# Kernel tuning notes

Measured on AMD Instinct MI355X. Metric: run time of the kernel, lower is better.

The kernel has to match this reference:

```python
import jax, jax.numpy as jnp
import numpy as np

TOP_K = 6  # num_experts_per_tok


def _glu_mlp(x, wg, wu, wd):
    # DeepSeek MLP: down( silu(gate(x)) * up(x) )
    return (jax.nn.silu(x @ wg) * (x @ wu)) @ wd


def setup_inputs() -> dict:
    key = jax.random.key(0)
    ks = jax.random.split(key, 8)
    B, S, D, E, F, FS = 2, 2048, 1024, 8, 512, 1024
    sc = 0.02
    return {
        "hidden_states": jax.random.normal(ks[0], (B, S, D), jnp.float32),
        "router_w": jax.random.normal(ks[1], (D, E), jnp.float32) * sc,
        "w_gate": jax.random.normal(ks[2], (E, D, F), jnp.float32) * sc,
        "w_up": jax.random.normal(ks[3], (E, D, F), jnp.float32) * sc,
        "w_down": jax.random.normal(ks[4], (E, F, D), jnp.float32) * sc,
        "ws_gate": jax.random.normal(ks[5], (D, FS), jnp.float32) * sc,
        "ws_up": jax.random.normal(ks[6], (D, FS), jnp.float32) * sc,
        "ws_down": jax.random.normal(ks[7], (FS, D), jnp.float32) * sc,
    }


def reference(hidden_states, router_w, w_gate, w_up, w_down, ws_gate, ws_up, ws_down):
    B, S, D = hidden_states.shape
    x = hidden_states.reshape(-1, D)                       # [T, D] tokens
    # Gate: softmax router + top-k (DeepSeek gate, no renorm)
    scores = jax.nn.softmax(x @ router_w, axis=-1)         # [T, E]
    topk_w, topk_idx = jax.lax.top_k(scores, TOP_K)        # [T, K]
    # Expert SiLU-GLU MLPs evaluated for all experts (math-identical to the
    # argsort dispatch -> grouped GEMM -> scatter combine in moe_infer)
    g = jnp.einsum('td,edf->etf', x, w_gate)               # [E, T, F]
    u = jnp.einsum('td,edf->etf', x, w_up)                 # [E, T, F]
    f_all = jnp.einsum('etf,efd->ted', jax.nn.silu(g) * u, w_down)  # [T, E, D]
    # Combine: final[t] = sum_k topk_w[t,k] * expert_{topk_idx[t,k]}(x[t])
    picked = jnp.take_along_axis(f_all, topk_idx[:, :, None], axis=1)  # [T, K, D]
    y = jnp.sum(picked * topk_w[:, :, None], axis=1).reshape(B, S, D)
    # shared experts branch
    y = y + _glu_mlp(hidden_states, ws_gate, ws_up, ws_down)
    return y
```

## Files before the change

### kernel.cpp

```cpp
#include <hip/hip_runtime.h>

typedef __attribute__((ext_vector_type(8))) short bf16x8;
typedef __attribute__((ext_vector_type(8))) unsigned short ushort8;
typedef __attribute__((ext_vector_type(4))) float floatx4;

static __device__ __forceinline__ unsigned short f2b(float f) {
  union { float f; unsigned int i; } v; v.f = f;
  unsigned int x = v.i;
  return (unsigned short)((x + 0x7fffu + ((x >> 16) & 1u)) >> 16);
}

#define GLDS(gp, lp) \
  __builtin_amdgcn_global_load_lds( \
      (const __attribute__((address_space(1))) unsigned int*)(gp), \
      (__attribute__((address_space(3))) unsigned int*)(lp), 16, 0, 0)

static __device__ __forceinline__ void swizzle_mn(int lin, int Mb, int Nb,
                                                  int& m_idx, int& n_idx) {
  if ((Mb & 7) == 0) {
    int xcd = lin & 7;
    int idx = lin >> 3;
    int nstrips = Mb >> 3;
    m_idx = (idx % nstrips) * 8 + xcd;
    n_idx = idx / nstrips;
  } else {
    m_idx = lin % Mb;
    n_idx = lin / Mb;
  }
}

__global__ __launch_bounds__(256) void router_cvt(
    const float* __restrict__ X, const float* __restrict__ RW,
    float* __restrict__ cw, unsigned short* __restrict__ Xb) {
  const int tid = threadIdx.x;
  const int wid = tid >> 6, lane = tid & 63;
  const int t = blockIdx.x * 4 + wid;
  const float* xp = X + (size_t)t * 1024;
  unsigned short* xo = Xb + (size_t)t * 1024;
  float acc[8];
#pragma unroll
  for (int e = 0; e < 8; e++) acc[e] = 0.f;
#pragma unroll
  for (int i = 0; i < 4; i++) {
    const int d0 = i * 256 + lane * 4;
    float4 v = *(const float4*)(xp + d0);
    ushort4 o;
    o.x = f2b(v.x); o.y = f2b(v.y); o.z = f2b(v.z); o.w = f2b(v.w);
    *(ushort4*)(xo + d0) = o;
    const float xv[4] = {v.x, v.y, v.z, v.w};
#pragma unroll
    for (int j = 0; j < 4; j++) {
      const float* r = RW + (size_t)(d0 + j) * 8;
      float4 r0 = *(const float4*)r;
      float4 r1 = *(const float4*)(r + 4);
      acc[0] += xv[j] * r0.x; acc[1] += xv[j] * r0.y;
      acc[2] += xv[j] * r0.z; acc[3] += xv[j] * r0.w;
      acc[4] += xv[j] * r1.x; acc[5] += xv[j] * r1.y;
      acc[6] += xv[j] * r1.z; acc[7] += xv[j] * r1.w;
    }
  }
#pragma unroll
  for (int m = 1; m < 64; m <<= 1) {
#pragma unroll
    for (int e = 0; e < 8; e++) acc[e] += __shfl_xor(acc[e], m);
  }
  if (lane == 0) {
    float mx = acc[0];
#pragma unroll
    for (int e = 1; e < 8; e++) mx = fmaxf(mx, acc[e]);
    float prob[8], s = 0.f;
#pragma unroll
    for (int e = 0; e < 8; e++) { prob[e] = expf(acc[e] - mx); s += prob[e]; }
    float inv = 1.f / s;
#pragma unroll
    for (int e = 0; e < 8; e++) prob[e] *= inv;
    int m1 = 0;
#pragma unroll
    for (int e = 1; e < 8; e++) if (prob[e] < prob[m1]) m1 = e;
    int m2 = -1;
#pragma unroll
    for (int e = 0; e < 8; e++)
      if (e != m1 && (m2 < 0 || prob[e] < prob[m2])) m2 = e;
#pragma unroll
    for (int e = 0; e < 8; e++)
      cw[(size_t)t * 8 + e] = (e == m1 || e == m2) ? 0.f : prob[e];
  }
}

__global__ __launch_bounds__(256) void transpose_all(
    const float* __restrict__ wg, const float* __restrict__ wu,
    const float* __restrict__ wd, const float* __restrict__ wsg,
    const float* __restrict__ wsu, const float* __restrict__ wsd,
    unsigned short* __restrict__ wgT, unsigned short* __restrict__ wuT,
    unsigned short* __restrict__ wdT, unsigned short* __restrict__ wsgT,
    unsigned short* __restrict__ wsuT, unsigned short* __restrict__ wsdT) {
  __shared__ __align__(16) unsigned short T[64 * 68];
  const int z = blockIdx.z;
  const float* src; unsigned short* dst; int K, N;
  if (z < 8)       { src = wg  + (size_t)z * 1024 * 512;        dst = wgT + (size_t)z * 512 * 1024;        K = 1024; N = 512; }
  else if (z < 16) { src = wu  + (size_t)(z - 8) * 1024 * 512;  dst = wuT + (size_t)(z - 8) * 512 * 1024;  K = 1024; N = 512; }
  else if (z < 24) { src = wd  + (size_t)(z - 16) * 512 * 1024; dst = wdT + (size_t)(z - 16) * 1024 * 512; K = 512;  N = 1024; }
  else if (z == 24){ src = wsg; dst = wsgT; K = 1024; N = 1024; }
  else if (z == 25){ src = wsu; dst = wsuT; K = 1024; N = 1024; }
  else             { src = wsd; dst = wsdT; K = 1024; N = 1024; }
  const int bn = blockIdx.x * 64, bk = blockIdx.y * 64;
  if (bn >= N || bk >= K) return;
  const int tid = threadIdx.x;
  {
    const int r = tid >> 4;
    const int c = (tid & 15) * 4;
#pragma unroll
    for (int i = 0; i < 4; i++) {
      const int rr = r + i * 16;
      float4 v = *(const float4*)(src + (size_t)(bk + rr) * N + bn + c);
      ushort4 o;
      o.x = f2b(v.x); o.y = f2b(v.y); o.z = f2b(v.z); o.w = f2b(v.w);
      *(ushort4*)(&T[rr * 68 + c]) = o;
    }
  }
  __syncthreads();
  {
    const int n_ = tid >> 3;
    const int k0 = (tid & 7) * 8;
#pragma unroll
    for (int p = 0; p < 2; p++) {
      const int n = n_ + p * 32;
      ushort8 o;
#pragma unroll
      for (int j = 0; j < 8; j++) o[j] = T[(k0 + j) * 68 + n];
      *(ushort8*)(dst + (size_t)(bn + n) * K + bk + k0) = o;
    }
  }
}

#define VMCNT(N) asm volatile("s_waitcnt vmcnt(" #N ")" ::: "memory")
#define BARS() do { __builtin_amdgcn_s_barrier(); \
                    __builtin_amdgcn_sched_barrier(0); } while (0)

#define STG_I0(K, BS) do { \
  GLDS(a0 + (K),          sm + (BS) + wid * 512); \
  GLDS(a0 + (K) + 131072, sm + (BS) + 8192 + wid * 512); } while (0)
#define STG_I1(K, BS) do { \
  GLDS(bg0 + (K),        sm + (BS) + 16384 + wid * 1024); \
  GLDS(bg0 + (K) + 8192, sm + (BS) + 16384 + wid * 1024 + 512); } while (0)
#define STG_I2(K, BS) do { \
  GLDS(bu0 + (K),        sm + (BS) + 24576 + wid * 1024); \
  GLDS(bu0 + (K) + 8192, sm + (BS) + 24576 + wid * 1024 + 512); } while (0)
#define STG_I3(K, BS) do { \
  GLDS(a0 + (K) + 65536,  sm + (BS) + 4096 + wid * 512); \
  GLDS(a0 + (K) + 196608, sm + (BS) + 12288 + wid * 512); } while (0)

#define READ_A(DST, DB, H) do { _Pragma("unroll") \
  for (int mf = 0; mf < 4; ++mf) { \
    const int row_ = wm * 128 + (H) * 64 + mf * 16 + lr; \
    const int rb_ = (DB) + row_ * 64; const int rx_ = row_ & 7; \
    DST[mf][0] = *(const bf16x8*)(sm + rb_ + ((quad ^ rx_) << 3)); \
    DST[mf][1] = *(const bf16x8*)(sm + rb_ + (((4 + quad) ^ rx_) << 3)); \
  } } while (0)

#define READ_B(DST, DB, RG) do { _Pragma("unroll") \
  for (int nf = 0; nf < 2; ++nf) { \
    const int row_ = wn * 32 + nf * 16 + lr; \
    const int rb_ = (DB) + (RG) + row_ * 64; const int rx_ = row_ & 7; \
    DST[nf][0] = *(const bf16x8*)(sm + rb_ + ((quad ^ rx_) << 3)); \
    DST[nf][1] = *(const bf16x8*)(sm + rb_ + (((4 + quad) ^ rx_) << 3)); \
  } } while (0)

#define MM(ACC, AF, BF) do { \
  __builtin_amdgcn_s_setprio(1); \
  _Pragma("unroll") \
  for (int mf = 0; mf < 4; ++mf) { _Pragma("unroll") \
    for (int nf = 0; nf < 2; ++nf) { \
      ACC[mf][nf] = __builtin_amdgcn_mfma_f32_16x16x32_bf16( \
          AF[mf][0], BF[nf][0], ACC[mf][nf], 0, 0, 0); \
      ACC[mf][nf] = __builtin_amdgcn_mfma_f32_16x16x32_bf16( \
          AF[mf][1], BF[nf][1], ACC[mf][nf], 0, 0, 0); \
    } } \
  __builtin_amdgcn_s_setprio(0); } while (0)

__global__ __launch_bounds__(512, 2) void gemm_gu_fused(
    const unsigned short* __restrict__ X,
    const unsigned short* __restrict__ WgTe,
    const unsigned short* __restrict__ WgTs,
    const unsigned short* __restrict__ WuTe,
    const unsigned short* __restrict__ WuTs,
    unsigned short* __restrict__ H,
    const float* __restrict__ cw, int Mb) {
  __shared__ __align__(16) unsigned short sm[65536];
  const int tid = threadIdx.x;
  const int wid = tid >> 6, lane = tid & 63;
  const int lr = lane & 15, quad = lane >> 4;
  const int wm = wid >> 2, wn = wid & 3;

  int m_idx, n_idx;
  {
    const int lin = blockIdx.x;
    const int xcd = lin & 7;
    const int idx = lin >> 3;
    m_idx = idx / 5;
    n_idx = xcd * 5 + (idx - m_idx * 5);
  }
  const int m0 = m_idx * 256;
  const int n0 = n_idx * 128;

  const unsigned short *Bg, *Bu;
  int eidx = -1;
  if (n0 < 4096) {
    eidx = n0 >> 9;
    size_t off = ((size_t)eidx * 512 + (n0 & 511)) * 1024;
    Bg = WgTe + off; Bu = WuTe + off;
  } else {
    size_t off = (size_t)(n0 - 4096) * 1024;
    Bg = WgTs + off; Bu = WuTs + off;
  }

  const int grow8 = lane >> 3;
  const int gcol = ((lane & 7) ^ grow8) << 3;
  const unsigned short* a0 =
      X + (size_t)(m0 + wid * 8 + grow8) * 1024 + gcol;
  const unsigned short* bg0 =
      Bg + (size_t)(wid * 16 + grow8) * 1024 + gcol;
  const unsigned short* bu0 =
      Bu + (size_t)(wid * 16 + grow8) * 1024 + gcol;

  floatx4 gg[2][4][2], uu[2][4][2];
#pragma unroll
  for (int h = 0; h < 2; h++)
#pragma unroll
    for (int mf = 0; mf < 4; mf++)
#pragma unroll
      for (int nf = 0; nf < 2; nf++) {
        gg[h][mf][nf] = (floatx4)0.f;
        uu[h][mf][nf] = (floatx4)0.f;
      }

  bf16x8 fA0[4][2], fA1[4][2], fBg[2][2], fBu[2][2];

  STG_I0(0, 0); STG_I1(0, 0); STG_I2(0, 0); STG_I3(0, 0);

  for (int t = 0; t < 15; ++t) {
    const int db = (t & 1) << 15;
    const int nb = 32768 - db;
    const int kn = (t + 1) * 64;
    STG_I0(kn, nb);
    VMCNT(6); BARS();
    READ_A(fA0, db, 0);
    READ_B(fBg, db, 16384);
    MM(gg[0], fA0, fBg);
    STG_I1(kn, nb);
    VMCNT(6); BARS();
    READ_B(fBu, db, 24576);
    MM(uu[0], fA0, fBu);
    STG_I2(kn, nb);
    VMCNT(6); BARS();
    READ_A(fA1, db, 1);
    MM(gg[1], fA1, fBg);
    STG_I3(kn, nb);
    BARS();
    MM(uu[1], fA1, fBu);
  }
  {
    const int db = 32768;
    VMCNT(4); BARS();
    READ_A(fA0, db, 0);
    READ_B(fBg, db, 16384);
    MM(gg[0], fA0, fBg);
    VMCNT(2); BARS();
    READ_B(fBu, db, 24576);
    MM(uu[0], fA0, fBu);
    VMCNT(0); BARS();
    READ_A(fA1, db, 1);
    MM(gg[1], fA1, fBg);
    MM(uu[1], fA1, fBu);
  }

#pragma unroll
  for (int h = 0; h < 2; h++) {
#pragma unroll
    for (int mf = 0; mf < 4; mf++) {
#pragma unroll
      for (int nf = 0; nf < 2; nf++) {
#pragma unroll
        for (int r = 0; r < 4; r++) {
          int row = m0 + wm * 128 + h * 64 + mf * 16 + quad * 4 + r;
          int col = n0 + wn * 32 + nf * 16 + lr;
          float g = gg[h][mf][nf][r];
          float u = uu[h][mf][nf][r];
          float s = (eidx >= 0) ? cw[(size_t)row * 8 + eidx] : 1.0f;
          float silu = g / (1.0f + __expf(-g));
          H[(size_t)row * 5120 + col] = f2b(s * silu * u);
        }
      }
    }
  }
}

#define DN_STG(KN, SBUF) do { \
  GLDS(Ha + (size_t)(KN),          smD + (SBUF) + wid * 512); \
  GLDS(Ha + (size_t)(KN) + 327680, smD + (SBUF) + 4096 + wid * 512); \
  const unsigned short *b0p_, *b1p_; \
  if ((KN) < 4096) { \
    const unsigned short* be_ = WdTe + ((size_t)((KN) >> 9)) * (1024 * 512) + ((KN) & 511); \
    b0p_ = be_ + (size_t)bn0 * 512 + gcol; \
    b1p_ = be_ + (size_t)(bn0 + 64) * 512 + gcol; \
  } else { \
    b0p_ = WdTs + (size_t)bn0 * 1024 + ((KN) - 4096) + gcol; \
    b1p_ = WdTs + (size_t)(bn0 + 64) * 1024 + ((KN) - 4096) + gcol; \
  } \
  GLDS(b0p_, smD + (SBUF) + 8192 + wid * 512); \
  GLDS(b1p_, smD + (SBUF) + 12288 + wid * 512); } while (0)

#define DN_TILE(T, BUF, SBUF, DOSTG, VM) do { \
  VMCNT(VM); BARS(); \
  if (DOSTG) { DN_STG(((T) + 3) * 64, SBUF); } \
  bf16x8 af_[4][2], bf_[2][2]; \
  _Pragma("unroll") \
  for (int mt = 0; mt < 4; ++mt) { \
    const int row_ = wm * 64 + mt * 16 + lr; \
    const int rb_ = (BUF) + row_ * 64; const int rx_ = row_ & 7; \
    af_[mt][0] = *(const bf16x8*)(smD + rb_ + ((quad ^ rx_) << 3)); \
    af_[mt][1] = *(const bf16x8*)(smD + rb_ + (((4 + quad) ^ rx_) << 3)); \
  } \
  _Pragma("unroll") \
  for (int nt = 0; nt < 2; ++nt) { \
    const int row_ = wn * 32 + nt * 16 + lr; \
    const int rb_ = (BUF) + 8192 + row_ * 64; const int rx_ = row_ & 7; \
    bf_[nt][0] = *(const bf16x8*)(smD + rb_ + ((quad ^ rx_) << 3)); \
    bf_[nt][1] = *(const bf16x8*)(smD + rb_ + (((4 + quad) ^ rx_) << 3)); \
  } \
  __builtin_amdgcn_s_setprio(1); \
  _Pragma("unroll") \
  for (int kt = 0; kt < 2; ++kt) \
    _Pragma("unroll") \
    for (int mt = 0; mt < 4; ++mt) \
      _Pragma("unroll") \
      for (int nt = 0; nt < 2; ++nt) \
        acc[mt][nt] = __builtin_amdgcn_mfma_f32_16x16x32_bf16( \
            af_[mt][kt], bf_[nt][kt], acc[mt][nt], 0, 0, 0); \
  __builtin_amdgcn_s_setprio(0); } while (0)

__global__ __launch_bounds__(512, 2) void gemm_down(
    const unsigned short* __restrict__ H,
    const unsigned short* __restrict__ WdTe,
    const unsigned short* __restrict__ WdTs,
    float* __restrict__ Y, int Mb) {
  __shared__ __align__(16) unsigned short smD[65536];
  const int tid = threadIdx.x;
  const int wid = tid >> 6, lane = tid & 63;
  const int lr = lane & 15, quad = lane >> 4;
  const int wm = wid >> 2, wn = wid & 3;
  int m_idx, n_idx;
  swizzle_mn(blockIdx.x, Mb, 8, m_idx, n_idx);
  const int m0 = m_idx * 128;
  const int n0 = n_idx * 128;

  const int grow8 = lane >> 3;
  const int gcol = ((lane & 7) ^ grow8) << 3;
  const unsigned short* Ha = H + (size_t)(m0 + wid * 8 + grow8) * 5120 + gcol;
  const int bn0 = n0 + wid * 8 + grow8;

  floatx4 acc[4][2];
#pragma unroll
  for (int i = 0; i < 4; i++)
#pragma unroll
    for (int j = 0; j < 2; j++) acc[i][j] = (floatx4)0.f;

  DN_STG(0, 0);
  DN_STG(64, 16384);
  DN_STG(128, 32768);

  for (int t = 0; t < 76; t += 4) {
    DN_TILE(t,     0,     49152, true, 8);
    DN_TILE(t + 1, 16384, 0,     true, 8);
    DN_TILE(t + 2, 32768, 16384, true, 8);
    DN_TILE(t + 3, 49152, 32768, true, 8);
  }
  DN_TILE(76, 0,     49152, true,  8);
  DN_TILE(77, 16384, 0,     false, 8);
  DN_TILE(78, 32768, 0,     false, 4);
  DN_TILE(79, 49152, 0,     false, 0);

#pragma unroll
  for (int mt = 0; mt < 4; mt++)
#pragma unroll
    for (int nt = 0; nt < 2; nt++)
#pragma unroll
      for (int r = 0; r < 4; r++) {
        int row = m0 + wm * 64 + mt * 16 + quad * 4 + r;
        int col = n0 + wn * 32 + nt * 16 + lr;
        Y[(size_t)row * 1024 + col] = acc[mt][nt][r];
      }
}

extern "C" void kernel_launch(void* const* d_in, const int* in_sizes, int n_in,
                              void* d_out, int out_size, void* d_ws, size_t ws_size,
                              hipStream_t stream) {
  const float* hs  = (const float*)d_in[0];
  const float* rw  = (const float*)d_in[1];
  const float* wg  = (const float*)d_in[2];
  const float* wu  = (const float*)d_in[3];
  const float* wd  = (const float*)d_in[4];
  const float* wsg = (const float*)d_in[5];
  const float* wsu = (const float*)d_in[6];
  const float* wsd = (const float*)d_in[7];
  float* out = (float*)d_out;

  char* p = (char*)d_ws;
  float* cw = (float*)p;                    p += (size_t)4096 * 8 * 4;
  unsigned short* Xb   = (unsigned short*)p; p += (size_t)4096 * 1024 * 2;
  unsigned short* wgT  = (unsigned short*)p; p += (size_t)8 * 512 * 1024 * 2;
  unsigned short* wuT  = (unsigned short*)p; p += (size_t)8 * 512 * 1024 * 2;
  unsigned short* wsgT = (unsigned short*)p; p += (size_t)1024 * 1024 * 2;
  unsigned short* wsuT = (unsigned short*)p; p += (size_t)1024 * 1024 * 2;
  unsigned short* wdT  = (unsigned short*)p; p += (size_t)8 * 1024 * 512 * 2;
  unsigned short* wsdT = (unsigned short*)p; p += (size_t)1024 * 1024 * 2;
  unsigned short* GH   = (unsigned short*)p;
  const size_t base_bytes = (size_t)(p - (char*)d_ws);

  int chunks = 8;
  for (int c = 1; c <= 8; c *= 2) {
    size_t gh_bytes = ((size_t)4096 / c) * 5120 * 2;
    if (base_bytes + gh_bytes <= ws_size) { chunks = c; break; }
  }
  const int rows = 4096 / chunks;
  const int Mb = rows / 128;
  const int MbG = rows / 256;

  router_cvt<<<1024, 256, 0, stream>>>(hs, rw, cw, Xb);
  transpose_all<<<dim3(16, 16, 27), 256, 0, stream>>>(
      wg, wu, wd, wsg, wsu, wsd, wgT, wuT, wdT, wsgT, wsuT, wsdT);

  for (int c = 0; c < chunks; c++) {
    const unsigned short* Xc = Xb + (size_t)c * rows * 1024;
    const float* cwc = cw + (size_t)c * rows * 8;
    float* outc = out + (size_t)c * rows * 1024;
    gemm_gu_fused<<<MbG * 40, 512, 0, stream>>>(
        Xc, wgT, wsgT, wuT, wsuT, GH, cwc, MbG);
    gemm_down<<<Mb * 8, 512, 0, stream>>>(GH, wdT, wsdT, outc, Mb);
  }
}
```

Baseline: 300.3 us.

## Split-K the down GEMM in two with atomic accumulation and smaller double buffer

The down-projection GEMM now splits its K=5120 reduction into two halves, doubling the grid, and accumulates the partial results into the output with float atomics after a zero-fill kernel. LDS use drops from a 4-stage to a 2-stage buffer, which allows 4 blocks per CU instead of 2. The aim is to fill the machine better when the tile grid is small. In exchange it adds an extra zeroing launch, atomic write traffic, a shallower prefetch pipeline and a non-deterministic summation order.

```diff
diff --git a/kernel.cpp b/kernel.cpp
--- a/kernel.cpp
+++ b/kernel.cpp
@@ -27,6 +27,11 @@
     m_idx = lin % Mb;
     n_idx = lin / Mb;
   }
+}
+
+__global__ void zero_f32(float* __restrict__ p) {
+  int i = (blockIdx.x * 256 + threadIdx.x) * 4;
+  *(float4*)(p + i) = make_float4(0.f, 0.f, 0.f, 0.f);
 }
 
 __global__ __launch_bounds__(256) void router_cvt(
@@ -310,49 +315,22 @@
   GLDS(b0p_, smD + (SBUF) + 8192 + wid * 512); \
   GLDS(b1p_, smD + (SBUF) + 12288 + wid * 512); } while (0)
 
-#define DN_TILE(T, BUF, SBUF, DOSTG, VM) do { \
-  VMCNT(VM); BARS(); \
-  if (DOSTG) { DN_STG(((T) + 3) * 64, SBUF); } \
-  bf16x8 af_[4][2], bf_[2][2]; \
-  _Pragma("unroll") \
-  for (int mt = 0; mt < 4; ++mt) { \
-    const int row_ = wm * 64 + mt * 16 + lr; \
-    const int rb_ = (BUF) + row_ * 64; const int rx_ = row_ & 7; \
-    af_[mt][0] = *(const bf16x8*)(smD + rb_ + ((quad ^ rx_) << 3)); \
-    af_[mt][1] = *(const bf16x8*)(smD + rb_ + (((4 + quad) ^ rx_) << 3)); \
-  } \
-  _Pragma("unroll") \
-  for (int nt = 0; nt < 2; ++nt) { \
-    const int row_ = wn * 32 + nt * 16 + lr; \
-    const int rb_ = (BUF) + 8192 + row_ * 64; const int rx_ = row_ & 7; \
-    bf_[nt][0] = *(const bf16x8*)(smD + rb_ + ((quad ^ rx_) << 3)); \
-    bf_[nt][1] = *(const bf16x8*)(smD + rb_ + (((4 + quad) ^ rx_) << 3)); \
-  } \
-  __builtin_amdgcn_s_setprio(1); \
-  _Pragma("unroll") \
-  for (int kt = 0; kt < 2; ++kt) \
-    _Pragma("unroll") \
-    for (int mt = 0; mt < 4; ++mt) \
-      _Pragma("unroll") \
-      for (int nt = 0; nt < 2; ++nt) \
-        acc[mt][nt] = __builtin_amdgcn_mfma_f32_16x16x32_bf16( \
-            af_[mt][kt], bf_[nt][kt], acc[mt][nt], 0, 0, 0); \
-  __builtin_amdgcn_s_setprio(0); } while (0)
-
-__global__ __launch_bounds__(512, 2) void gemm_down(
+__global__ __launch_bounds__(512, 4) void gemm_down(
     const unsigned short* __restrict__ H,
     const unsigned short* __restrict__ WdTe,
     const unsigned short* __restrict__ WdTs,
     float* __restrict__ Y, int Mb) {
-  __shared__ __align__(16) unsigned short smD[65536];
+  __shared__ __align__(16) unsigned short smD[32768];
   const int tid = threadIdx.x;
   const int wid = tid >> 6, lane = tid & 63;
   const int lr = lane & 15, quad = lane >> 4;
   const int wm = wid >> 2, wn = wid & 3;
+  const int s = blockIdx.x & 1;
   int m_idx, n_idx;
-  swizzle_mn(blockIdx.x, Mb, 8, m_idx, n_idx);
+  swizzle_mn(blockIdx.x >> 1, Mb, 8, m_idx, n_idx);
   const int m0 = m_idx * 128;
   const int n0 = n_idx * 128;
+  const int t0 = s * 40;
 
   const int grow8 = lane >> 3;
   const int gcol = ((lane & 7) ^ grow8) << 3;
@@ -365,20 +343,45 @@
 #pragma unroll
     for (int j = 0; j < 2; j++) acc[i][j] = (floatx4)0.f;
 
-  DN_STG(0, 0);
-  DN_STG(64, 16384);
-  DN_STG(128, 32768);
-
-  for (int t = 0; t < 76; t += 4) {
-    DN_TILE(t,     0,     49152, true, 8);
-    DN_TILE(t + 1, 16384, 0,     true, 8);
-    DN_TILE(t + 2, 32768, 16384, true, 8);
-    DN_TILE(t + 3, 49152, 32768, true, 8);
-  }
-  DN_TILE(76, 0,     49152, true,  8);
-  DN_TILE(77, 16384, 0,     false, 8);
-  DN_TILE(78, 32768, 0,     false, 4);
-  DN_TILE(79, 49152, 0,     false, 0);
+  DN_STG(t0 * 64, 0);
+
+  for (int tt = 0; tt < 40; ++tt) {
+    const int db = (tt & 1) * 16384;
+    const int nb = 16384 - db;
+    if (tt < 39) {
+      DN_STG((t0 + tt + 1) * 64, nb);
+      VMCNT(4);
+    } else {
+      VMCNT(0);
+    }
+    BARS();
+    bf16x8 af_[4][2], bf_[2][2];
+#pragma unroll
+    for (int mt = 0; mt < 4; ++mt) {
+      const int row_ = wm * 64 + mt * 16 + lr;
+      const int rb_ = db + row_ * 64; const int rx_ = row_ & 7;
+      af_[mt][0] = *(const bf16x8*)(smD + rb_ + ((quad ^ rx_) << 3));
+      af_[mt][1] = *(const bf16x8*)(smD + rb_ + (((4 + quad) ^ rx_) << 3));
+    }
+#pragma unroll
+    for (int nt = 0; nt < 2; ++nt) {
+      const int row_ = wn * 32 + nt * 16 + lr;
+      const int rb_ = db + 8192 + row_ * 64; const int rx_ = row_ & 7;
+      bf_[nt][0] = *(const bf16x8*)(smD + rb_ + ((quad ^ rx_) << 3));
+      bf_[nt][1] = *(const bf16x8*)(smD + rb_ + (((4 + quad) ^ rx_) << 3));
+    }
+    __builtin_amdgcn_s_setprio(1);
+#pragma unroll
+    for (int kt = 0; kt < 2; ++kt)
+#pragma unroll
+      for (int mt = 0; mt < 4; ++mt)
+#pragma unroll
+        for (int nt = 0; nt < 2; ++nt)
+          acc[mt][nt] = __builtin_amdgcn_mfma_f32_16x16x32_bf16(
+              af_[mt][kt], bf_[nt][kt], acc[mt][nt], 0, 0, 0);
+    __builtin_amdgcn_s_setprio(0);
+    BARS();
+  }
 
 #pragma unroll
   for (int mt = 0; mt < 4; mt++)
@@ -388,7 +391,7 @@
       for (int r = 0; r < 4; r++) {
         int row = m0 + wm * 64 + mt * 16 + quad * 4 + r;
         int col = n0 + wn * 32 + nt * 16 + lr;
-        Y[(size_t)row * 1024 + col] = acc[mt][nt][r];
+        unsafeAtomicAdd(&Y[(size_t)row * 1024 + col], acc[mt][nt][r]);
       }
 }
 
@@ -434,8 +437,9 @@
     const unsigned short* Xc = Xb + (size_t)c * rows * 1024;
     const float* cwc = cw + (size_t)c * rows * 8;
     float* outc = out + (size_t)c * rows * 1024;
+    zero_f32<<<rows, 256, 0, stream>>>(outc);
     gemm_gu_fused<<<MbG * 40, 512, 0, stream>>>(
         Xc, wgT, wsgT, wuT, wsuT, GH, cwc, MbG);
-    gemm_down<<<Mb * 8, 512, 0, stream>>>(GH, wdT, wsdT, outc, Mb);
-  }
-}
+    gemm_down<<<Mb * 16, 512, 0, stream>>>(GH, wdT, wsdT, outc, Mb);
+  }
+}
```

Result: slower. 323.5 us (+7.7%).
